# Performance work log

Hardware: AMD Instinct MI355X
Metric: run time of the kernel (lower is better)

The kernel has to match this reference:

```python
import jax, jax.numpy as jnp
import numpy as np

B, N, C, H, E = 16, 512, 128, 8, 131072
Nn = B * N
Dh = C // H
EPS = 1e-5


def setup_inputs() -> dict:
    key = jax.random.key(0)
    ks = jax.random.split(key, 16)
    s = C ** -0.5
    x = jax.random.normal(ks[0], (Nn, C), dtype=jnp.float32)
    edge_index = jax.random.randint(ks[1], (2, E), 0, Nn)
    batch = jnp.arange(Nn) // N  # B equal-sized graphs, sorted
    attn_bias = jax.random.normal(ks[2], (B, N, N, H), dtype=jnp.float32)
    return {
        "x": x,
        "edge_index": edge_index,
        "batch": batch,
        "attn_bias": attn_bias,
        "conv_w": jax.random.normal(ks[3], (C, C)) * s,
        "conv_b": jnp.zeros((C,)),
        "wq": jax.random.normal(ks[4], (C, C)) * s,
        "bq": jnp.zeros((C,)),
        "wk": jax.random.normal(ks[5], (C, C)) * s,
        "bk": jnp.zeros((C,)),
        "wv": jax.random.normal(ks[6], (C, C)) * s,
        "bv": jnp.zeros((C,)),
        "wo": jax.random.normal(ks[7], (C, C)) * s,
        "bo": jnp.zeros((C,)),
        "w1": jax.random.normal(ks[8], (C, 2 * C)) * s,
        "b1": jnp.zeros((2 * C,)),
        "w2": jax.random.normal(ks[9], (2 * C, C)) * (2 * C) ** -0.5,
        "b2": jnp.zeros((C,)),
        "g1": jnp.ones((C,)), "be1": jnp.zeros((C,)),
        "g2": jnp.ones((C,)), "be2": jnp.zeros((C,)),
        "g3": jnp.ones((C,)), "be3": jnp.zeros((C,)),
    }


def _bn(h, g, b):
    # BatchNorm1d over the node dimension (training-mode batch statistics)
    mu = h.mean(axis=0)
    var = h.var(axis=0)  # biased, matches torch normalization
    return g * (h - mu) * jax.lax.rsqrt(var + EPS) + b


def reference(x, edge_index, batch, attn_bias,
              conv_w, conv_b, wq, bq, wk, bk, wv, bv, wo, bo,
              w1, b1, w2, b2, g1, be1, g2, be2, g3, be3):
    n_nodes, ch = x.shape
    bsz, n_max, _, heads = attn_bias.shape
    dh = ch // heads

    # ---- GCN conv (self loops + symmetric norm) -> dropout(0) + residual + norm1
    loops = jnp.arange(n_nodes)
    src = jnp.concatenate([edge_index[0], loops])
    dst = jnp.concatenate([edge_index[1], loops])
    deg = jax.ops.segment_sum(jnp.ones_like(src, dtype=x.dtype), dst, num_segments=n_nodes)
    dinv = jax.lax.rsqrt(jnp.maximum(deg, 1.0))
    xw = x @ conv_w
    msg = xw[src] * (dinv[src] * dinv[dst])[:, None]
    hconv = jax.ops.segment_sum(msg, dst, num_segments=n_nodes) + conv_b
    h1 = _bn(hconv + x, g1, be1)

    # ---- dense batch (equal-sized sorted graphs -> pure reshape, mask all-valid)
    xd = x.reshape(bsz, n_max, ch)
    q = ((xd @ wq + bq) * (dh ** -0.5)).reshape(bsz, n_max, heads, dh)
    k = (xd @ wk + bk).reshape(bsz, n_max, heads, dh)
    v = (xd @ wv + bv).reshape(bsz, n_max, heads, dh)
    scores = jnp.einsum('bqhd,bkhd->bqkh', q, k) + attn_bias  # [B,N,N,H]
    probs = jax.nn.softmax(scores, axis=2)
    att = jnp.einsum('bqkh,bkhd->bqhd', probs, v).reshape(bsz, n_max, ch)
    att = att @ wo + bo
    h2 = _bn(att.reshape(n_nodes, ch) + x, g2, be2)

    # ---- combine branches, MLP with residual, norm3
    out = h1 + h2
    mlp = jax.nn.relu(out @ w1 + b1) @ w2 + b2
    return _bn(out + mlp, g3, be3)
```

## Files before the change

### kernel.cpp

```cpp
#include <hip/hip_runtime.h>
#include <cstddef>

#define NN 8192
#define CC 128

static __device__ inline unsigned f2bf_pack(float a, float b) {
  unsigned ua = __builtin_bit_cast(unsigned, a);
  ua += 0x7fffu + ((ua >> 16) & 1u);
  unsigned ub = __builtin_bit_cast(unsigned, b);
  ub += 0x7fffu + ((ub >> 16) & 1u);
  return (ua >> 16) | (ub & 0xffff0000u);
}
static __device__ inline float bf_lo(unsigned u) { return __builtin_bit_cast(float, u << 16); }
static __device__ inline float bf_hi(unsigned u) { return __builtin_bit_cast(float, u & 0xffff0000u); }


__global__ __launch_bounds__(256) void count_deg_int_k(const int* __restrict__ dst, int* degi, int E) {
  int i = blockIdx.x * 256 + threadIdx.x;
  if (i < E) atomicAdd(&degi[dst[i]], 1);
}

__global__ __launch_bounds__(256) void dinv_k(const int* __restrict__ degi, float* __restrict__ dinv, int n) {
  int i = blockIdx.x * 256 + threadIdx.x;
  if (i < n) dinv[i] = rsqrtf((float)(degi[i] + 1));
}

__global__ __launch_bounds__(256) void scan_k(const int* __restrict__ degi, int* __restrict__ rowstart,
                                              int* __restrict__ cursor) {
  __shared__ int partial[256];
  int t = threadIdx.x;
  int base = t * 32;
  int local[32];
  int s = 0;
#pragma unroll
  for (int i = 0; i < 32; ++i) { local[i] = s; s += degi[base + i]; }
  partial[t] = s;
  __syncthreads();
  for (int off = 1; off < 256; off <<= 1) {
    int v = (t >= off) ? partial[t - off] : 0;
    __syncthreads();
    partial[t] += v;
    __syncthreads();
  }
  int offset = partial[t] - s;
#pragma unroll
  for (int i = 0; i < 32; ++i) {
    rowstart[base + i] = offset + local[i];
    cursor[base + i] = offset + local[i];
  }
  if (t == 255) rowstart[NN] = offset + s;
}

__global__ __launch_bounds__(256) void bucket_k(const int* __restrict__ src, const int* __restrict__ dst,
    int* __restrict__ cursor, int* __restrict__ col, int E) {
  int e = blockIdx.x * 256 + threadIdx.x;
  if (e >= E) return;
  int d = dst[e];
  int pos = atomicAdd(&cursor[d], 1);
  col[pos] = src[e];
}

__global__ __launch_bounds__(256) void gather_k(const int* __restrict__ rowstart, const int* __restrict__ col,
    const float* __restrict__ xws, const float* __restrict__ dinv, const float* __restrict__ cb,
    const float* __restrict__ x, float* __restrict__ h1) {
  int d = blockIdx.x * 2 + (threadIdx.x >> 7);
  int c = threadIdx.x & 127;
  int j0 = rowstart[d], j1 = rowstart[d + 1];
  float dd = dinv[d];
  float sum = 0.f;
  float v = 0.f;
  if (j0 < j1) v = xws[(size_t)col[j0] * CC + c];
  for (int j = j0; j < j1; ++j) {
    float v_next = 0.f;
    if (j + 1 < j1) v_next = xws[(size_t)col[j + 1] * CC + c];
    sum += v;
    v = v_next;
  }
  int idx = d * CC + c;
  sum += xws[idx];
  h1[idx] = sum * dd + cb[c] + x[idx];
}


__global__ __launch_bounds__(256) void bn_stats_k(const float* __restrict__ X,
    float* __restrict__ sums, float* __restrict__ sumsq) {
  int t = threadIdx.x;
  int c = t & 127, rg = t >> 7;
  int r0 = blockIdx.x * 64;
  float s = 0.f, sq = 0.f;
  for (int i = 0; i < 32; ++i) {
    float v = X[(size_t)(r0 + rg + 2 * i) * CC + c];
    s += v; sq += v * v;
  }
  atomicAdd(&sums[c], s);
  atomicAdd(&sumsq[c], sq);
}

__global__ __launch_bounds__(256) void combine_k(const float* __restrict__ h1, const float* __restrict__ h2,
    const float* __restrict__ st, const float* __restrict__ g1, const float* __restrict__ be1,
    const float* __restrict__ g2, const float* __restrict__ be2, float* __restrict__ out) {
  int idx = blockIdx.x * 256 + threadIdx.x;
  int c = idx & 127;
  float mu1 = st[c] * (1.f / NN);
  float var1 = st[128 + c] * (1.f / NN) - mu1 * mu1;
  float sc1 = g1[c] * rsqrtf(var1 + 1e-5f);
  float sh1 = be1[c] - mu1 * sc1;
  float mu2 = st[256 + c] * (1.f / NN);
  float var2 = st[384 + c] * (1.f / NN) - mu2 * mu2;
  float sc2 = g2[c] * rsqrtf(var2 + 1e-5f);
  float sh2 = be2[c] - mu2 * sc2;
  out[idx] = sc1 * h1[idx] + sh1 + sc2 * h2[idx] + sh2;
}

__global__ __launch_bounds__(256) void bn_apply_k(const float* __restrict__ h, const float* __restrict__ st,
    const float* __restrict__ g3, const float* __restrict__ be3, float* __restrict__ out) {
  int idx = blockIdx.x * 256 + threadIdx.x;
  int c = idx & 127;
  float mu = st[512 + c] * (1.f / NN);
  float var = st[640 + c] * (1.f / NN) - mu * mu;
  float sc = g3[c] * rsqrtf(var + 1e-5f);
  float sh = be3[c] - mu * sc;
  out[idx] = sc * h[idx] + sh;
}

__global__ __launch_bounds__(256) void gemm_k(const float* __restrict__ A, const float* __restrict__ W,
    const float* __restrict__ bias, const float* __restrict__ resid, const float* __restrict__ dscale,
    float* __restrict__ out, int M, int N, int K, float scale, int relu) {
  __shared__ float As[64 * 132];
  __shared__ float Ws[128 * 64];
  int t = threadIdx.x;
  int ty = t >> 4, tx = t & 15;
  int row0 = blockIdx.x * 64, n0 = blockIdx.y * 64;
  float acc[4][4] = {};
  for (int kc = 0; kc < K; kc += 128) {
#pragma unroll
    for (int j = 0; j < 8; ++j) {
      int f = t + 256 * j;
      int r = f >> 5, c4 = f & 31;
      *(float4*)(As + r * 132 + c4 * 4) = *(const float4*)(A + (size_t)(row0 + r) * K + kc + c4 * 4);
    }
#pragma unroll
    for (int j = 0; j < 8; ++j) {
      int f = t + 256 * j;
      int kr = f >> 4, c4 = f & 15;
      *(float4*)(Ws + kr * 64 + c4 * 4) = *(const float4*)(W + (size_t)(kc + kr) * N + n0 + c4 * 4);
    }
    __syncthreads();
    for (int k0 = 0; k0 < 128; k0 += 4) {
      float a[4][4], b[4][4];
#pragma unroll
      for (int i = 0; i < 4; ++i) {
        float4 t4 = *(const float4*)(As + (4 * ty + i) * 132 + k0);
        a[i][0] = t4.x; a[i][1] = t4.y; a[i][2] = t4.z; a[i][3] = t4.w;
      }
#pragma unroll
      for (int kk = 0; kk < 4; ++kk) {
        float4 t4 = *(const float4*)(Ws + (k0 + kk) * 64 + 4 * tx);
        b[kk][0] = t4.x; b[kk][1] = t4.y; b[kk][2] = t4.z; b[kk][3] = t4.w;
      }
#pragma unroll
      for (int kk = 0; kk < 4; ++kk)
#pragma unroll
        for (int i = 0; i < 4; ++i)
#pragma unroll
          for (int j = 0; j < 4; ++j)
            acc[i][j] += a[i][kk] * b[kk][j];
    }
    __syncthreads();
  }
  float4 bv = make_float4(0.f, 0.f, 0.f, 0.f);
  if (bias) bv = *(const float4*)(bias + n0 + 4 * tx);
#pragma unroll
  for (int i = 0; i < 4; ++i) {
    int row = row0 + 4 * ty + i;
    float ds = dscale ? dscale[row] : 1.f;
    float4 r;
    r.x = (acc[i][0] + bv.x) * scale * ds;
    r.y = (acc[i][1] + bv.y) * scale * ds;
    r.z = (acc[i][2] + bv.z) * scale * ds;
    r.w = (acc[i][3] + bv.w) * scale * ds;
    if (relu) { r.x = fmaxf(r.x, 0.f); r.y = fmaxf(r.y, 0.f); r.z = fmaxf(r.z, 0.f); r.w = fmaxf(r.w, 0.f); }
    size_t o = (size_t)row * N + n0 + 4 * tx;
    if (resid) {
      float4 rv = *(const float4*)(resid + o);
      r.x += rv.x; r.y += rv.y; r.z += rv.z; r.w += rv.w;
    }
    *(float4*)(out + o) = r;
  }
}

#define ROWS 160
__global__ __launch_bounds__(64, 2) void attn_k(const float* __restrict__ Q, const float* __restrict__ K,
    const float* __restrict__ V, const float* __restrict__ bias,
    unsigned* __restrict__ pA, unsigned* __restrict__ pB, float* __restrict__ lbuf) {
  __shared__ float Ks[8 * ROWS];
  __shared__ float Vs[8 * ROWS];
  __shared__ float Bs[32 * 65];
  const int t = threadIdx.x;
  const int b = blockIdx.x >> 4;
  const int qt = blockIdx.x & 15;
  const int s = blockIdx.y;
  const int qq = t >> 3;
  const int h = t & 7;
  const int node_t = b * 512 + qt * 32;
  const int node0 = node_t + qq * 4;

  float qf[4][16];
#pragma unroll
  for (int r = 0; r < 4; ++r) {
    const float4* qp = (const float4*)(Q + (size_t)(node0 + r) * CC + h * 16);
#pragma unroll
    for (int i = 0; i < 4; ++i) {
      float4 a = qp[i];
      qf[r][4*i] = a.x; qf[r][4*i+1] = a.y; qf[r][4*i+2] = a.z; qf[r][4*i+3] = a.w;
    }
  }
  float l[4] = {0.f, 0.f, 0.f, 0.f};
  float acc[4][16];
#pragma unroll
  for (int r = 0; r < 4; ++r)
#pragma unroll
    for (int d = 0; d < 16; ++d) acc[r][d] = 0.f;

  const int key0 = s * 128;
  const size_t kvb = (size_t)b * 512 * CC + (size_t)key0 * CC;
  const float* bbase = bias + ((size_t)node_t * 512 + key0) * 8;

  float4 kst[4], vst[4], bst[8];

#pragma unroll
  for (int j = 0; j < 4; ++j) {
    int f = t + 64 * j;
    int row = f >> 5, c4 = f & 31;
    size_t go = kvb + (size_t)row * CC + c4 * 4;
    kst[j] = *(const float4*)(K + go);
    vst[j] = *(const float4*)(V + go);
  }
#pragma unroll
  for (int j = 0; j < 8; ++j) {
    int f = t + 64 * j;
    int q = f >> 4, f4 = f & 15;
    bst[j] = *(const float4*)(bbase + (size_t)q * 4096 + f4 * 4);
  }
#pragma unroll
  for (int j = 0; j < 4; ++j) {
    int f = t + 64 * j;
    int row = f >> 5, c4 = f & 31;
    int lo = row * ROWS + (c4 >> 2) * 20 + (c4 & 3) * 4;
    *(float4*)(Ks + lo) = kst[j];
    *(float4*)(Vs + lo) = vst[j];
  }
#pragma unroll
  for (int j = 0; j < 8; ++j) {
    int f = t + 64 * j;
    int q = f >> 4, f4 = f & 15;
    *(float4*)(Bs + q * 65 + f4 * 4) = bst[j];
  }

  for (int ch = 0; ch < 16; ++ch) {
    if (ch + 1 < 16) {
#pragma unroll
      for (int j = 0; j < 4; ++j) {
        int f = t + 64 * j;
        int row = f >> 5, c4 = f & 31;
        size_t go = kvb + (size_t)((ch + 1) * 8 + row) * CC + c4 * 4;
        kst[j] = *(const float4*)(K + go);
        vst[j] = *(const float4*)(V + go);
      }
#pragma unroll
      for (int j = 0; j < 8; ++j) {
        int f = t + 64 * j;
        int q = f >> 4, f4 = f & 15;
        bst[j] = *(const float4*)(bbase + (size_t)q * 4096 + (ch + 1) * 64 + f4 * 4);
      }
    }
#pragma unroll 2
    for (int kk = 0; kk < 8; ++kk) {
      const float4* kf = (const float4*)(Ks + kk * ROWS + h * 20);
      float4 k0 = kf[0], k1 = kf[1], k2 = kf[2], k3 = kf[3];
      const float4* vf = (const float4*)(Vs + kk * ROWS + h * 20);
      float4 v0 = vf[0], v1 = vf[1], v2 = vf[2], v3 = vf[3];
#pragma unroll
      for (int r = 0; r < 4; ++r) {
        float sc = Bs[(qq * 4 + r) * 65 + kk * 8 + h];
        sc += qf[r][0] * k0.x + qf[r][1] * k0.y + qf[r][2] * k0.z + qf[r][3] * k0.w
            + qf[r][4] * k1.x + qf[r][5] * k1.y + qf[r][6] * k1.z + qf[r][7] * k1.w
            + qf[r][8] * k2.x + qf[r][9] * k2.y + qf[r][10] * k2.z + qf[r][11] * k2.w
            + qf[r][12] * k3.x + qf[r][13] * k3.y + qf[r][14] * k3.z + qf[r][15] * k3.w;
        float p = __expf(sc);
        l[r] += p;
        acc[r][0] += p * v0.x; acc[r][1] += p * v0.y; acc[r][2] += p * v0.z; acc[r][3] += p * v0.w;
        acc[r][4] += p * v1.x; acc[r][5] += p * v1.y; acc[r][6] += p * v1.z; acc[r][7] += p * v1.w;
        acc[r][8] += p * v2.x; acc[r][9] += p * v2.y; acc[r][10] += p * v2.z; acc[r][11] += p * v2.w;
        acc[r][12] += p * v3.x; acc[r][13] += p * v3.y; acc[r][14] += p * v3.z; acc[r][15] += p * v3.w;
      }
    }
    if (ch + 1 < 16) {
#pragma unroll
      for (int j = 0; j < 4; ++j) {
        int f = t + 64 * j;
        int row = f >> 5, c4 = f & 31;
        int lo = row * ROWS + (c4 >> 2) * 20 + (c4 & 3) * 4;
        *(float4*)(Ks + lo) = kst[j];
        *(float4*)(Vs + lo) = vst[j];
      }
#pragma unroll
      for (int j = 0; j < 8; ++j) {
        int f = t + 64 * j;
        int q = f >> 4, f4 = f & 15;
        *(float4*)(Bs + q * 65 + f4 * 4) = bst[j];
      }
    }
  }

  unsigned* pbase = (s < 2 ? pA : pB) + (size_t)(s & 1) * (NN * CC / 2);
#pragma unroll
  for (int r = 0; r < 4; ++r) {
    int slot = ((node0 + r) * 8 + h) * 8;
    unsigned u[8];
#pragma unroll
    for (int j = 0; j < 8; ++j) u[j] = f2bf_pack(acc[r][2*j], acc[r][2*j+1]);
    *(uint4*)(pbase + slot)     = make_uint4(u[0], u[1], u[2], u[3]);
    *(uint4*)(pbase + slot + 4) = make_uint4(u[4], u[5], u[6], u[7]);
    lbuf[s * 65536 + (node0 + r) * 8 + h] = l[r];
  }
}

__global__ __launch_bounds__(256) void attn_merge_k(const unsigned* __restrict__ pA,
    const unsigned* __restrict__ pB, const float* __restrict__ lbuf, float* __restrict__ out) {
  int i = blockIdx.x * 256 + threadIdx.x;
  float L = lbuf[i] + lbuf[65536 + i] + lbuf[131072 + i] + lbuf[196608 + i];
  float inv = 1.f / L;
  float o[16];
#pragma unroll
  for (int d = 0; d < 16; ++d) o[d] = 0.f;
#pragma unroll
  for (int s = 0; s < 4; ++s) {
    const unsigned* pb = (s < 2 ? pA : pB) + (size_t)(s & 1) * (NN * CC / 2) + (size_t)i * 8;
    uint4 a = *(const uint4*)pb;
    uint4 b = *(const uint4*)(pb + 4);
    unsigned u[8] = {a.x, a.y, a.z, a.w, b.x, b.y, b.z, b.w};
#pragma unroll
    for (int j = 0; j < 8; ++j) {
      o[2*j]   += bf_lo(u[j]);
      o[2*j+1] += bf_hi(u[j]);
    }
  }
  float* po = out + (size_t)i * 16;
#pragma unroll
  for (int j = 0; j < 4; ++j)
    *(float4*)(po + 4 * j) = make_float4(o[4*j] * inv, o[4*j+1] * inv, o[4*j+2] * inv, o[4*j+3] * inv);
}


extern "C" void kernel_launch(void* const* d_in, const int* in_sizes, int n_in,
                              void* d_out, int out_size, void* d_ws, size_t ws_size,
                              hipStream_t stream) {
  const float* x      = (const float*)d_in[0];
  const int*   ei     = (const int*)d_in[1];
  const float* bias   = (const float*)d_in[3];
  const float* conv_w = (const float*)d_in[4];
  const float* conv_b = (const float*)d_in[5];
  const float* wq = (const float*)d_in[6];
  const float* bq = (const float*)d_in[7];
  const float* wk = (const float*)d_in[8];
  const float* bk = (const float*)d_in[9];
  const float* wv = (const float*)d_in[10];
  const float* bv = (const float*)d_in[11];
  const float* wo = (const float*)d_in[12];
  const float* bo = (const float*)d_in[13];
  const float* w1 = (const float*)d_in[14];
  const float* b1 = (const float*)d_in[15];
  const float* w2 = (const float*)d_in[16];
  const float* b2 = (const float*)d_in[17];
  const float* g1 = (const float*)d_in[18];
  const float* be1 = (const float*)d_in[19];
  const float* g2 = (const float*)d_in[20];
  const float* be2 = (const float*)d_in[21];
  const float* g3 = (const float*)d_in[22];
  const float* be3 = (const float*)d_in[23];
  int E = in_sizes[1] / 2;

  float* ws = (float*)d_ws;
  const size_t NC = (size_t)NN * CC;
  float* xw     = ws;
  float* h1pre  = ws + NC;
  float* qb     = ws + 2 * NC;
  float* kb     = ws + 3 * NC;
  float* vb     = ws + 4 * NC;
  float* h2pre  = ws + 5 * NC;
  float* outbuf = ws + 6 * NC;
  float* hid    = ws + 2 * NC;
  float* h3pre  = ws + 4 * NC;
  float* st     = ws + 7 * NC;
  float* dinv   = ws + 7 * NC + 768;
  int*   degi     = (int*)(ws + 7 * NC + 768 + NN);
  int*   rowstart = degi + NN;
  int*   cursor   = rowstart + NN + 1;
  int*   col      = cursor + NN;
  float* lbuf     = (float*)(col + E);

  hipMemsetAsync(degi, 0, NN * sizeof(int), stream);
  hipMemsetAsync(st, 0, 768 * sizeof(float), stream);

  count_deg_int_k<<<(E + 255) / 256, 256, 0, stream>>>(ei + E, degi, E);
  dinv_k<<<NN / 256, 256, 0, stream>>>(degi, dinv, NN);
  scan_k<<<1, 256, 0, stream>>>(degi, rowstart, cursor);
  bucket_k<<<(E + 255) / 256, 256, 0, stream>>>(ei, ei + E, cursor, col, E);
  gemm_k<<<dim3(NN / 64, 2), 256, 0, stream>>>(x, conv_w, nullptr, nullptr, dinv, xw, NN, CC, CC, 1.f, 0);
  gather_k<<<NN / 2, 256, 0, stream>>>(rowstart, col, xw, dinv, conv_b, x, h1pre);
  bn_stats_k<<<NN / 64, 256, 0, stream>>>(h1pre, st + 0, st + 128);

  gemm_k<<<dim3(NN / 64, 2), 256, 0, stream>>>(x, wq, bq, nullptr, nullptr, qb, NN, CC, CC, 0.25f, 0);
  gemm_k<<<dim3(NN / 64, 2), 256, 0, stream>>>(x, wk, bk, nullptr, nullptr, kb, NN, CC, CC, 1.f, 0);
  gemm_k<<<dim3(NN / 64, 2), 256, 0, stream>>>(x, wv, bv, nullptr, nullptr, vb, NN, CC, CC, 1.f, 0);
  attn_k<<<dim3(256, 4), 64, 0, stream>>>(qb, kb, vb, bias, (unsigned*)xw, (unsigned*)h2pre, lbuf);
  attn_merge_k<<<65536 / 256, 256, 0, stream>>>((unsigned*)xw, (unsigned*)h2pre, lbuf, outbuf);
  gemm_k<<<dim3(NN / 64, 2), 256, 0, stream>>>(outbuf, wo, bo, x, nullptr, h2pre, NN, CC, CC, 1.f, 0);
  bn_stats_k<<<NN / 64, 256, 0, stream>>>(h2pre, st + 256, st + 384);

  combine_k<<<NC / 256, 256, 0, stream>>>(h1pre, h2pre, st, g1, be1, g2, be2, outbuf);
  gemm_k<<<dim3(NN / 64, 4), 256, 0, stream>>>(outbuf, w1, b1, nullptr, nullptr, hid, NN, 2 * CC, CC, 1.f, 1);
  gemm_k<<<dim3(NN / 64, 2), 256, 0, stream>>>(hid, w2, b2, outbuf, nullptr, h3pre, NN, CC, 2 * CC, 1.f, 0);
  bn_stats_k<<<NN / 64, 256, 0, stream>>>(h3pre, st + 512, st + 640);
  bn_apply_k<<<NC / 256, 256, 0, stream>>>(h3pre, st, g3, be3, (float*)d_out);
}
```

Baseline: 498.8 us.

## Stage attention K/V/bias tiles via direct global-to-LDS loads with double buffering

Replaces the register-staged K/V/bias prefetch in the attention kernel with global_load_lds transfers into a double-buffered shared tile, using vmcnt waits instead of register round-trips. The LDS layout changes to unpadded rows, with a rotated float4 order per head and a rotated bias layout to avoid bank conflicts, and the output store is permuted to match. It frees the registers that held the prefetch, but doubles LDS use and drops the launch bound from two blocks per CU to one, which may lower occupancy. There is also no workgroup barrier between buffer reuse, which relies on each 64-thread block being a single wavefront.

```diff
diff --git a/kernel.cpp b/kernel.cpp
--- a/kernel.cpp
+++ b/kernel.cpp
@@ -13,6 +13,12 @@
 }
 static __device__ inline float bf_lo(unsigned u) { return __builtin_bit_cast(float, u << 16); }
 static __device__ inline float bf_hi(unsigned u) { return __builtin_bit_cast(float, u & 0xffff0000u); }
+
+typedef const __attribute__((address_space(1))) void gvoid_t;
+typedef __attribute__((address_space(3))) void lvoid_t;
+static __device__ inline void glds16(const float* g, float* l) {
+  __builtin_amdgcn_global_load_lds((gvoid_t*)g, (lvoid_t*)l, 16, 0, 0);
+}
 
 
 __global__ __launch_bounds__(256) void count_deg_int_k(const int* __restrict__ dst, int* degi, int E) {
@@ -189,13 +195,10 @@
   }
 }
 
-#define ROWS 160
-__global__ __launch_bounds__(64, 2) void attn_k(const float* __restrict__ Q, const float* __restrict__ K,
+__global__ __launch_bounds__(64, 1) void attn_k(const float* __restrict__ Q, const float* __restrict__ K,
     const float* __restrict__ V, const float* __restrict__ bias,
     unsigned* __restrict__ pA, unsigned* __restrict__ pB, float* __restrict__ lbuf) {
-  __shared__ float Ks[8 * ROWS];
-  __shared__ float Vs[8 * ROWS];
-  __shared__ float Bs[32 * 65];
+  __shared__ float SM[2][4096];
   const int t = threadIdx.x;
   const int b = blockIdx.x >> 4;
   const int qt = blockIdx.x & 15;
@@ -204,111 +207,81 @@
   const int h = t & 7;
   const int node_t = b * 512 + qt * 32;
   const int node0 = node_t + qq * 4;
-
-  float qf[4][16];
-#pragma unroll
-  for (int r = 0; r < 4; ++r) {
-    const float4* qp = (const float4*)(Q + (size_t)(node0 + r) * CC + h * 16);
+  const int key0 = s * 128;
+  const size_t kvb = ((size_t)b * 512 + key0) * CC;
+  const float* bbase = bias + ((size_t)node_t * 512 + key0) * 8;
+
+  float4 qf[4][4];
+#pragma unroll
+  for (int r = 0; r < 4; ++r)
+#pragma unroll
+    for (int j = 0; j < 4; ++j)
+      qf[r][j] = *(const float4*)(Q + (size_t)(node0 + r) * CC + h * 16 + (((j + h) & 3) << 2));
+
+  float4 acc[4][4];
+  float l[4] = {0.f, 0.f, 0.f, 0.f};
+#pragma unroll
+  for (int r = 0; r < 4; ++r)
+#pragma unroll
+    for (int j = 0; j < 4; ++j) acc[r][j] = make_float4(0.f, 0.f, 0.f, 0.f);
+
+  auto stage = [&](int ch, int bf) {
+    const float* kg = K + kvb + ch * 1024;
+    const float* vg = V + kvb + ch * 1024;
+    float* ksl = &SM[bf][0];
+    float* vsl = &SM[bf][1024];
+    float* bsl = &SM[bf][2048];
 #pragma unroll
     for (int i = 0; i < 4; ++i) {
-      float4 a = qp[i];
-      qf[r][4*i] = a.x; qf[r][4*i+1] = a.y; qf[r][4*i+2] = a.z; qf[r][4*i+3] = a.w;
-    }
-  }
-  float l[4] = {0.f, 0.f, 0.f, 0.f};
-  float acc[4][16];
-#pragma unroll
-  for (int r = 0; r < 4; ++r)
-#pragma unroll
-    for (int d = 0; d < 16; ++d) acc[r][d] = 0.f;
-
-  const int key0 = s * 128;
-  const size_t kvb = (size_t)b * 512 * CC + (size_t)key0 * CC;
-  const float* bbase = bias + ((size_t)node_t * 512 + key0) * 8;
-
-  float4 kst[4], vst[4], bst[8];
-
-#pragma unroll
-  for (int j = 0; j < 4; ++j) {
-    int f = t + 64 * j;
-    int row = f >> 5, c4 = f & 31;
-    size_t go = kvb + (size_t)row * CC + c4 * 4;
-    kst[j] = *(const float4*)(K + go);
-    vst[j] = *(const float4*)(V + go);
-  }
-#pragma unroll
-  for (int j = 0; j < 8; ++j) {
-    int f = t + 64 * j;
-    int q = f >> 4, f4 = f & 15;
-    bst[j] = *(const float4*)(bbase + (size_t)q * 4096 + f4 * 4);
-  }
-#pragma unroll
-  for (int j = 0; j < 4; ++j) {
-    int f = t + 64 * j;
-    int row = f >> 5, c4 = f & 31;
-    int lo = row * ROWS + (c4 >> 2) * 20 + (c4 & 3) * 4;
-    *(float4*)(Ks + lo) = kst[j];
-    *(float4*)(Vs + lo) = vst[j];
-  }
-#pragma unroll
-  for (int j = 0; j < 8; ++j) {
-    int f = t + 64 * j;
-    int q = f >> 4, f4 = f & 15;
-    *(float4*)(Bs + q * 65 + f4 * 4) = bst[j];
-  }
-
+      glds16(kg + i * 256 + t * 4, ksl + i * 256);
+      glds16(vg + i * 256 + t * 4, vsl + i * 256);
+    }
+#pragma unroll
+    for (int i = 0; i < 8; ++i) {
+      int g = i * 64 + t;
+      int q = g >> 4;
+      int kkp = (g >> 1) & 7;
+      int hq = g & 1;
+      int kk = (kkp - (q >> 2)) & 7;
+      glds16(bbase + (size_t)q * 4096 + (ch * 8 + kk) * 8 + hq * 4, bsl + i * 256);
+    }
+  };
+
+  stage(0, 0);
   for (int ch = 0; ch < 16; ++ch) {
-    if (ch + 1 < 16) {
-#pragma unroll
-      for (int j = 0; j < 4; ++j) {
-        int f = t + 64 * j;
-        int row = f >> 5, c4 = f & 31;
-        size_t go = kvb + (size_t)((ch + 1) * 8 + row) * CC + c4 * 4;
-        kst[j] = *(const float4*)(K + go);
-        vst[j] = *(const float4*)(V + go);
-      }
-#pragma unroll
-      for (int j = 0; j < 8; ++j) {
-        int f = t + 64 * j;
-        int q = f >> 4, f4 = f & 15;
-        bst[j] = *(const float4*)(bbase + (size_t)q * 4096 + (ch + 1) * 64 + f4 * 4);
-      }
-    }
+    int bf = ch & 1;
+    if (ch + 1 < 16) stage(ch + 1, bf ^ 1);
+    asm volatile("" ::: "memory");
+    if (ch + 1 < 16) __builtin_amdgcn_s_waitcnt(0x4F70);
+    else             __builtin_amdgcn_s_waitcnt(0x0F70);
+    asm volatile("" ::: "memory");
+    const float* ksl = &SM[bf][0];
+    const float* vsl = &SM[bf][1024];
+    const float* bsl = &SM[bf][2048];
 #pragma unroll 2
     for (int kk = 0; kk < 8; ++kk) {
-      const float4* kf = (const float4*)(Ks + kk * ROWS + h * 20);
-      float4 k0 = kf[0], k1 = kf[1], k2 = kf[2], k3 = kf[3];
-      const float4* vf = (const float4*)(Vs + kk * ROWS + h * 20);
-      float4 v0 = vf[0], v1 = vf[1], v2 = vf[2], v3 = vf[3];
+      float4 kr[4], vr[4];
+#pragma unroll
+      for (int j = 0; j < 4; ++j) {
+        int off = kk * 128 + h * 16 + (((j + h) & 3) << 2);
+        kr[j] = *(const float4*)(ksl + off);
+        vr[j] = *(const float4*)(vsl + off);
+      }
+      int brot = ((kk + qq) & 7) << 3;
 #pragma unroll
       for (int r = 0; r < 4; ++r) {
-        float sc = Bs[(qq * 4 + r) * 65 + kk * 8 + h];
-        sc += qf[r][0] * k0.x + qf[r][1] * k0.y + qf[r][2] * k0.z + qf[r][3] * k0.w
-            + qf[r][4] * k1.x + qf[r][5] * k1.y + qf[r][6] * k1.z + qf[r][7] * k1.w
-            + qf[r][8] * k2.x + qf[r][9] * k2.y + qf[r][10] * k2.z + qf[r][11] * k2.w
-            + qf[r][12] * k3.x + qf[r][13] * k3.y + qf[r][14] * k3.z + qf[r][15] * k3.w;
+        float sc = bsl[(qq * 4 + r) * 64 + brot + h];
+#pragma unroll
+        for (int j = 0; j < 4; ++j)
+          sc += qf[r][j].x * kr[j].x + qf[r][j].y * kr[j].y
+              + qf[r][j].z * kr[j].z + qf[r][j].w * kr[j].w;
         float p = __expf(sc);
         l[r] += p;
-        acc[r][0] += p * v0.x; acc[r][1] += p * v0.y; acc[r][2] += p * v0.z; acc[r][3] += p * v0.w;
-        acc[r][4] += p * v1.x; acc[r][5] += p * v1.y; acc[r][6] += p * v1.z; acc[r][7] += p * v1.w;
-        acc[r][8] += p * v2.x; acc[r][9] += p * v2.y; acc[r][10] += p * v2.z; acc[r][11] += p * v2.w;
-        acc[r][12] += p * v3.x; acc[r][13] += p * v3.y; acc[r][14] += p * v3.z; acc[r][15] += p * v3.w;
-      }
-    }
-    if (ch + 1 < 16) {
-#pragma unroll
-      for (int j = 0; j < 4; ++j) {
-        int f = t + 64 * j;
-        int row = f >> 5, c4 = f & 31;
-        int lo = row * ROWS + (c4 >> 2) * 20 + (c4 & 3) * 4;
-        *(float4*)(Ks + lo) = kst[j];
-        *(float4*)(Vs + lo) = vst[j];
-      }
-#pragma unroll
-      for (int j = 0; j < 8; ++j) {
-        int f = t + 64 * j;
-        int q = f >> 4, f4 = f & 15;
-        *(float4*)(Bs + q * 65 + f4 * 4) = bst[j];
+#pragma unroll
+        for (int j = 0; j < 4; ++j) {
+          acc[r][j].x += p * vr[j].x; acc[r][j].y += p * vr[j].y;
+          acc[r][j].z += p * vr[j].z; acc[r][j].w += p * vr[j].w;
+        }
       }
     }
   }
@@ -317,11 +290,13 @@
 #pragma unroll
   for (int r = 0; r < 4; ++r) {
     int slot = ((node0 + r) * 8 + h) * 8;
-    unsigned u[8];
-#pragma unroll
-    for (int j = 0; j < 8; ++j) u[j] = f2bf_pack(acc[r][2*j], acc[r][2*j+1]);
-    *(uint4*)(pbase + slot)     = make_uint4(u[0], u[1], u[2], u[3]);
-    *(uint4*)(pbase + slot + 4) = make_uint4(u[4], u[5], u[6], u[7]);
+#pragma unroll
+    for (int j = 0; j < 4; ++j) {
+      int g = (j + h) & 3;
+      unsigned u0 = f2bf_pack(acc[r][j].x, acc[r][j].y);
+      unsigned u1 = f2bf_pack(acc[r][j].z, acc[r][j].w);
+      *(uint2*)(pbase + slot + g * 2) = make_uint2(u0, u1);
+    }
     lbuf[s * 65536 + (node0 + r) * 8 + h] = l[r];
   }
 }
```

Result: faster. 442.2 us (-11.3%).
